# Kernel tuning notes

Hardware: AMD Instinct MI355X
Metric: run time of the kernel (lower is better)

Reference implementation:

```python
import jax, jax.numpy as jnp
import numpy as np

COMMITMENT = 0.25
THRESHOLD = 0.6
SNR_DB = 30.0  # eval_snr_db default-ish channel condition (fixed for determinism)
LN_EPS = 1e-5


def _layernorm(x, g, b):
    m = jnp.mean(x, axis=-1, keepdims=True)
    v = jnp.var(x, axis=-1, keepdims=True)
    return (x - m) * jax.lax.rsqrt(v + LN_EPS) * g + b


def _vq(x, codebook):
    # x: [T, D], codebook: [K, D]. Nearest-neighbor quantize + per-token VQ loss + STE.
    d = (x * x).sum(-1, keepdims=True) - 2.0 * (x @ codebook.T) + (codebook * codebook).sum(-1)  # [T, K]
    idx = jnp.argmin(d, axis=-1)
    q = codebook[idx]  # [T, D]
    loss = (COMMITMENT * jnp.mean((x - jax.lax.stop_gradient(q)) ** 2, axis=-1)
            + jnp.mean((jax.lax.stop_gradient(x) - q) ** 2, axis=-1))  # [T]
    q_ste = x + jax.lax.stop_gradient(q - x)
    return q_ste, loss


def setup_inputs() -> dict:
    key = jax.random.key(0)
    ks = jax.random.split(key, 8)
    B, N, De, Dq, Dd = 64, 196, 768, 512, 256
    return {
        'x_tokens': jax.random.normal(ks[0], (B, N, De), jnp.float32),
        'fim_logits': jax.random.normal(ks[1], (B, N, 1), jnp.float32),
        'W_proj': jax.random.normal(ks[2], (De, Dq), jnp.float32) * (1.0 / np.sqrt(De)),
        'b_proj': jnp.zeros((Dq,), jnp.float32),
        'ln_g': jnp.ones((Dq,), jnp.float32),
        'ln_b': jnp.zeros((Dq,), jnp.float32),
        'cb_high': jax.random.normal(ks[3], (4096, Dq), jnp.float32),
        'cb_low': jax.random.normal(ks[4], (256, Dq), jnp.float32),
        'W_dec': jax.random.normal(ks[5], (Dq, Dd), jnp.float32) * (1.0 / np.sqrt(Dq)),
        'b_dec': jnp.zeros((Dd,), jnp.float32),
        'h_ri': jax.random.normal(ks[6], (B, 2), jnp.float32),
        'noise': jax.random.normal(ks[7], (B, N, Dq), jnp.float32),
    }


def reference(x_tokens, fim_logits, W_proj, b_proj, ln_g, ln_b, cb_high, cb_low, W_dec, b_dec, h_ri, noise):
    B, N, _ = x_tokens.shape
    score = jax.nn.sigmoid(fim_logits[..., 0])          # [B, N]
    route_high = score > THRESHOLD                       # [B, N] bool

    x_proj = _layernorm(x_tokens @ W_proj + b_proj, ln_g, ln_b)  # [B, N, Dq]
    D = x_proj.shape[-1]
    xf = x_proj.reshape(-1, D)
    mf = route_high.reshape(-1)
    sf = score.reshape(-1)

    # Compute both experts densely, select with mask (same math as the masked
    # gather/scatter dispatch in the torch code, jit-friendly static shapes).
    q_high, loss_high = _vq(xf, cb_high)
    q_low, loss_low = _vq(xf, cb_low)
    final = jnp.where(mf[:, None], q_high, q_low).reshape(B, N, D)

    n_high = jnp.maximum(mf.sum(), 1)
    n_low = jnp.maximum((~mf).sum(), 1)
    vq_loss = (jnp.sum(jnp.where(mf, loss_high * sf, 0.0)) / n_high
               + jnp.sum(jnp.where(mf, 0.0, loss_low * (1.0 - sf))) / n_low) / 2.0

    # Rayleigh channel: per-sample fading magnitude h = |CN(0,1)|/sqrt(2), AWGN, equalize.
    n_var = 10.0 ** (-SNR_DB / 10.0)
    h = jnp.sqrt((h_ri ** 2).sum(-1)) / jnp.sqrt(2.0)    # [B]
    h = h[:, None, None]
    y = (h * final + jnp.sqrt(n_var) * noise) / h

    x_dec = y @ W_dec + b_dec                            # [B, N, 256]
    return x_dec, vq_loss
```

## Files before the change

kernel.cpp:

```cpp
#include <hip/hip_runtime.h>
#include <math.h>

#define T_TOK 12544
#define DE 768
#define DQ 512
#define DD 256
#define SEQ 196
#define NCH 4096
#define NCL 256
#define SPL_H 16
#define CODES_PER_BLK 256
#define MARGIN 2.0f
#define CAND_CAP 16
#define VQTOK 32

typedef __attribute__((ext_vector_type(8))) short s16x8;
typedef __attribute__((ext_vector_type(4))) float f32x4;

__device__ __forceinline__ float wave_reduce_sum(float v) {
    #pragma unroll
    for (int off = 32; off > 0; off >>= 1) v += __shfl_xor(v, off);
    return v;
}

__device__ __forceinline__ unsigned short f2bf(float f) {
    unsigned int u = __float_as_uint(f);
    u = (u + 0x7fffu + ((u >> 16) & 1u)) >> 16;
    return (unsigned short)u;
}
__device__ __forceinline__ float bf2f(unsigned short h) {
    return __uint_as_float(((unsigned int)h) << 16);
}

__device__ __forceinline__ void gload_lds16(const unsigned short* g, unsigned short* l) {
    __builtin_amdgcn_global_load_lds(
        (const __attribute__((address_space(1))) void*)g,
        (__attribute__((address_space(3))) void*)l,
        16, 0, 0);
}

__device__ __forceinline__ void sumsq_body(const float* __restrict__ cb,
                                           float* __restrict__ cs2,
                                           unsigned short* __restrict__ cbB,
                                           int blk, int NC) {
    int row = blk * 4 + (threadIdx.x >> 6);
    int lane = threadIdx.x & 63;
    if (row >= NC) return;
    const float4* p = (const float4*)(cb + (size_t)row * DQ);
    float4 a = p[lane];
    float4 b = p[lane + 64];
    if (cbB) {
        unsigned short* dst = cbB + (size_t)row * DQ;
        ushort4 ha, hb;
        ha.x = f2bf(a.x); ha.y = f2bf(a.y); ha.z = f2bf(a.z); ha.w = f2bf(a.w);
        hb.x = f2bf(b.x); hb.y = f2bf(b.y); hb.z = f2bf(b.z); hb.w = f2bf(b.w);
        *(ushort4*)(dst + lane * 4) = ha;
        *(ushort4*)(dst + 256 + lane * 4) = hb;
    }
    float s = a.x*a.x + a.y*a.y + a.z*a.z + a.w*a.w
            + b.x*b.x + b.y*b.y + b.z*b.z + b.w*b.w;
    s = wave_reduce_sum(s);
    if (lane == 0) cs2[row] = s;
}

__device__ __forceinline__ void split_body(const float* __restrict__ W, int K, int N,
                                           unsigned short* __restrict__ Thi,
                                           unsigned short* __restrict__ Tlo,
                                           int blk, int nb) {
    int total = K * N;
    for (int idx = blk * 256 + threadIdx.x; idx < total; idx += nb * 256) {
        int n = idx / K, k = idx - n * K;
        float v = W[(size_t)k * N + n];
        unsigned short h = f2bf(v);
        Thi[idx] = h;
        Tlo[idx] = f2bf(v - bf2f(h));
    }
}

__global__ __launch_bounds__(256) void prep_all(const float* __restrict__ cb_h,
                                                float* __restrict__ cs2h,
                                                unsigned short* __restrict__ cbhB,
                                                const float* __restrict__ cb_l,
                                                float* __restrict__ cs2l,
                                                unsigned short* __restrict__ cblB,
                                                const float* __restrict__ Wp,
                                                unsigned short* __restrict__ WThi,
                                                unsigned short* __restrict__ WTlo,
                                                const float* __restrict__ Wd,
                                                unsigned short* __restrict__ WdThi,
                                                unsigned short* __restrict__ WdTlo,
                                                int* __restrict__ counts) {
    int blk = blockIdx.x;
    if (blk == 0 && threadIdx.x == 0) { counts[0] = 0; counts[1] = 0; }
    if (blk < 1024)       sumsq_body(cb_h, cs2h, cbhB, blk, NCH);
    else if (blk < 1088)  sumsq_body(cb_l, cs2l, cblB, blk - 1024, NCL);
    else if (blk < 1600)  split_body(Wp, DE, DQ, WThi, WTlo, blk - 1088, 512);
    else                  split_body(Wd, DQ, DD, WdThi, WdTlo, blk - 1600, 256);
}

template<int NC>
__global__ __launch_bounds__(256) void code_sumsq(const float* __restrict__ cb,
                                                  float* __restrict__ cs2) {
    sumsq_body(cb, cs2, nullptr, blockIdx.x, NC);
}

template<int KDIM, int NSTRIDE>
__global__ __launch_bounds__(256) void gemm_mfma3_128(const float* __restrict__ A,
                                                      const unsigned short* __restrict__ BThi,
                                                      const unsigned short* __restrict__ BTlo,
                                                      const float* __restrict__ bias,
                                                      float* __restrict__ out) {
    __shared__ __align__(16) unsigned short Ahi[128 * 32];
    __shared__ __align__(16) unsigned short Alo[128 * 32];
    __shared__ __align__(16) unsigned short Bhi[128 * 32];
    __shared__ __align__(16) unsigned short Blo[128 * 32];
    const int m0 = blockIdx.x * 128, n0 = blockIdx.y * 128;
    const int tid = threadIdx.x, lane = tid & 63, w = tid >> 6;
    const int wr = w >> 1, wc = w & 1;
    const int arow = tid >> 1, ahalf = tid & 1;

    const int cb0 = w * 2, cb1 = w * 2 + 1;
    const int gcol0 = n0 + cb0 * 16 + (lane >> 2);
    const int gcol1 = n0 + cb1 * 16 + (lane >> 2);
    const int ch0 = (lane & 3) ^ ((gcol0 >> 1) & 3);
    const int ch1 = (lane & 3) ^ ((gcol1 >> 1) & 3);
    const unsigned short* sH0 = BThi + (size_t)gcol0 * KDIM + ch0 * 8;
    const unsigned short* sH1 = BThi + (size_t)gcol1 * KDIM + ch1 * 8;
    const unsigned short* sL0 = BTlo + (size_t)gcol0 * KDIM + ch0 * 8;
    const unsigned short* sL1 = BTlo + (size_t)gcol1 * KDIM + ch1 * 8;

    f32x4 acc[4][4] = {};
    const int NT = KDIM / 32;
    for (int t = 0; t < NT; t++) {
        const int k0 = t * 32;
        gload_lds16(sH0 + k0, Bhi + cb0 * 512);
        gload_lds16(sH1 + k0, Bhi + cb1 * 512);
        gload_lds16(sL0 + k0, Blo + cb0 * 512);
        gload_lds16(sL1 + k0, Blo + cb1 * 512);
        {
            const float* src = A + (size_t)(m0 + arow) * KDIM + k0 + ahalf * 16;
            float4 v0 = *(const float4*)(src + 0);
            float4 v1 = *(const float4*)(src + 4);
            float4 v2 = *(const float4*)(src + 8);
            float4 v3 = *(const float4*)(src + 12);
            float xv[16] = {v0.x,v0.y,v0.z,v0.w, v1.x,v1.y,v1.z,v1.w,
                            v2.x,v2.y,v2.z,v2.w, v3.x,v3.y,v3.z,v3.w};
            const int swzA = (arow >> 1) & 3;
            #pragma unroll
            for (int cc = 0; cc < 2; cc++) {
                unsigned int hw[4], lw[4];
                #pragma unroll
                for (int j = 0; j < 4; j++) {
                    float f0 = xv[cc*8 + 2*j], f1 = xv[cc*8 + 2*j + 1];
                    unsigned short h0 = f2bf(f0), h1 = f2bf(f1);
                    unsigned short l0 = f2bf(f0 - bf2f(h0));
                    unsigned short l1 = f2bf(f1 - bf2f(h1));
                    hw[j] = (unsigned)h0 | ((unsigned)h1 << 16);
                    lw[j] = (unsigned)l0 | ((unsigned)l1 << 16);
                }
                int c = ahalf * 2 + cc;
                int doff = arow * 32 + (c ^ swzA) * 8;
                *(uint4*)&Ahi[doff] = make_uint4(hw[0], hw[1], hw[2], hw[3]);
                *(uint4*)&Alo[doff] = make_uint4(lw[0], lw[1], lw[2], lw[3]);
            }
        }
        __syncthreads();
        const int fr = lane & 15, fs = lane >> 4;
        s16x8 ah[4], al[4];
        #pragma unroll
        for (int tm = 0; tm < 4; tm++) {
            int row = wr * 64 + tm * 16 + fr;
            int off = row * 32 + (fs ^ ((row >> 1) & 3)) * 8;
            ah[tm] = *(const s16x8*)&Ahi[off];
            al[tm] = *(const s16x8*)&Alo[off];
        }
        #pragma unroll
        for (int tn = 0; tn < 4; tn++) {
            int col = wc * 64 + tn * 16 + fr;
            int boff = col * 32 + (fs ^ ((col >> 1) & 3)) * 8;
            s16x8 bh = *(const s16x8*)&Bhi[boff];
            s16x8 bl = *(const s16x8*)&Blo[boff];
            #pragma unroll
            for (int tm = 0; tm < 4; tm++) {
                acc[tm][tn] = __builtin_amdgcn_mfma_f32_16x16x32_bf16(ah[tm], bh, acc[tm][tn], 0, 0, 0);
                acc[tm][tn] = __builtin_amdgcn_mfma_f32_16x16x32_bf16(ah[tm], bl, acc[tm][tn], 0, 0, 0);
                acc[tm][tn] = __builtin_amdgcn_mfma_f32_16x16x32_bf16(al[tm], bh, acc[tm][tn], 0, 0, 0);
            }
        }
        __syncthreads();
    }
    const int fr = lane & 15, fg = lane >> 4;
    #pragma unroll
    for (int tn = 0; tn < 4; tn++) {
        const int col = n0 + wc * 64 + tn * 16 + fr;
        const float bb = bias[col];
        #pragma unroll
        for (int tm = 0; tm < 4; tm++) {
            #pragma unroll
            for (int r = 0; r < 4; r++) {
                int row = m0 + wr * 64 + tm * 16 + fg * 4 + r;
                out[(size_t)row * NSTRIDE + col] = acc[tm][tn][r] + bb;
            }
        }
    }
}

__global__ __launch_bounds__(256) void dec_mfma3_loss(const float* __restrict__ A,
                                                      const unsigned short* __restrict__ BThi,
                                                      const unsigned short* __restrict__ BTlo,
                                                      const float* __restrict__ bias,
                                                      float* __restrict__ out,
                                                      const float* __restrict__ lh,
                                                      const float* __restrict__ ll,
                                                      const int* __restrict__ counts) {
    __shared__ __align__(16) unsigned short Ahi[2][64 * 32];
    __shared__ __align__(16) unsigned short Alo[2][64 * 32];
    __shared__ __align__(16) unsigned short Bhi[2][64 * 32];
    __shared__ __align__(16) unsigned short Blo[2][64 * 32];
    if (blockIdx.x == T_TOK / 64) {
        if (blockIdx.y != 0) return;
        float* sh = (float*)&Ahi[0][0];
        float* sl = sh + 256;
        int tid = threadIdx.x;
        float ah = 0.f, al = 0.f;
        for (int t = tid; t < T_TOK; t += 256) { ah += lh[t]; al += ll[t]; }
        sh[tid] = ah; sl[tid] = al;
        __syncthreads();
        for (int o = 128; o > 0; o >>= 1) {
            if (tid < o) { sh[tid] += sh[tid + o]; sl[tid] += sl[tid + o]; }
            __syncthreads();
        }
        if (tid == 0) {
            int nh = counts[0];
            int nl = T_TOK - nh;
            nh = nh > 1 ? nh : 1;
            nl = nl > 1 ? nl : 1;
            out[(size_t)T_TOK * DD] = 0.5f * (sh[0] / (float)nh + sl[0] / (float)nl);
        }
        return;
    }
    const int m0 = blockIdx.x * 64, n0 = blockIdx.y * 64;
    const int tid = threadIdx.x, lane = tid & 63, w = tid >> 6;
    const int stok = tid >> 2, sslot = tid & 3;

    f32x4 acc[4] = {};
    float4 av0, av1;
    uint4 bh4, bl4;

    auto loadStep = [&](int k0) {
        const float* src = A + (size_t)(m0 + stok) * DQ + k0 + sslot * 8;
        av0 = *(const float4*)src;
        av1 = *(const float4*)(src + 4);
        size_t soff = (size_t)(n0 + stok) * DQ + k0 + sslot * 8;
        bh4 = *(const uint4*)(BThi + soff);
        bl4 = *(const uint4*)(BTlo + soff);
    };
    auto writeStep = [&](int buf) {
        float xv[8] = {av0.x, av0.y, av0.z, av0.w, av1.x, av1.y, av1.z, av1.w};
        unsigned int hw[4], lw[4];
        #pragma unroll
        for (int j = 0; j < 4; j++) {
            unsigned short h0 = f2bf(xv[2*j]),   h1 = f2bf(xv[2*j+1]);
            unsigned short l0 = f2bf(xv[2*j] - bf2f(h0));
            unsigned short l1 = f2bf(xv[2*j+1] - bf2f(h1));
            hw[j] = (unsigned)h0 | ((unsigned)h1 << 16);
            lw[j] = (unsigned)l0 | ((unsigned)l1 << 16);
        }
        int doffA = stok * 32 + (sslot ^ ((stok >> 1) & 3)) * 8;
        *(uint4*)&Ahi[buf][doffA] = make_uint4(hw[0], hw[1], hw[2], hw[3]);
        *(uint4*)&Alo[buf][doffA] = make_uint4(lw[0], lw[1], lw[2], lw[3]);
        *(uint4*)&Bhi[buf][doffA] = bh4;
        *(uint4*)&Blo[buf][doffA] = bl4;
    };

    loadStep(0); writeStep(0); __syncthreads();
    const int NT = DQ / 32;
    for (int t = 0; t < NT; t++) {
        const int cur = t & 1;
        if (t + 1 < NT) loadStep((t + 1) * 32);
        const int fr = lane & 15, fs = lane >> 4;
        s16x8 ah[4], al[4];
        #pragma unroll
        for (int tm = 0; tm < 4; tm++) {
            int tok = tm * 16 + fr;
            int off = tok * 32 + (fs ^ ((tok >> 1) & 3)) * 8;
            ah[tm] = *(const s16x8*)&Ahi[cur][off];
            al[tm] = *(const s16x8*)&Alo[cur][off];
        }
        {
            int col = w * 16 + fr;
            int boff = col * 32 + (fs ^ ((col >> 1) & 3)) * 8;
            s16x8 bh = *(const s16x8*)&Bhi[cur][boff];
            s16x8 bl = *(const s16x8*)&Blo[cur][boff];
            #pragma unroll
            for (int tm = 0; tm < 4; tm++) {
                acc[tm] = __builtin_amdgcn_mfma_f32_16x16x32_bf16(ah[tm], bh, acc[tm], 0, 0, 0);
                acc[tm] = __builtin_amdgcn_mfma_f32_16x16x32_bf16(ah[tm], bl, acc[tm], 0, 0, 0);
                acc[tm] = __builtin_amdgcn_mfma_f32_16x16x32_bf16(al[tm], bh, acc[tm], 0, 0, 0);
            }
        }
        if (t + 1 < NT) writeStep(cur ^ 1);
        __syncthreads();
    }
    const int fr = lane & 15, fg = lane >> 4;
    {
        const int col = n0 + w * 16 + fr;
        const float bb = bias[col];
        #pragma unroll
        for (int tm = 0; tm < 4; tm++) {
            #pragma unroll
            for (int r = 0; r < 4; r++) {
                int row = m0 + tm * 16 + fg * 4 + r;
                out[(size_t)row * DD + col] = acc[tm][r] + bb;
            }
        }
    }
}

__global__ __launch_bounds__(256) void proj_gemm(const float* __restrict__ X,
                                                 const float* __restrict__ W,
                                                 const float* __restrict__ bias,
                                                 float* __restrict__ out) {
    __shared__ float As[32][66];
    __shared__ float Bs[32][64];
    const int m0 = blockIdx.x * 64, n0 = blockIdx.y * 64;
    const int tid = threadIdx.x;
    const int tx = tid & 15, ty = tid >> 4;
    float acc[4][4] = {};
    for (int k0 = 0; k0 < DE; k0 += 32) {
        {
            int e = tid;
            int r = e >> 3, c4 = e & 7;
            float4 v = *(const float4*)(X + (size_t)(m0 + r) * DE + k0 + c4 * 4);
            As[c4*4+0][r] = v.x; As[c4*4+1][r] = v.y; As[c4*4+2][r] = v.z; As[c4*4+3][r] = v.w;
            e = tid + 256;
            r = e >> 3; c4 = e & 7;
            v = *(const float4*)(X + (size_t)(m0 + r) * DE + k0 + c4 * 4);
            As[c4*4+0][r] = v.x; As[c4*4+1][r] = v.y; As[c4*4+2][r] = v.z; As[c4*4+3][r] = v.w;
        }
        {
            int e = tid;
            int kk = e >> 4, c4 = e & 15;
            *(float4*)&Bs[kk][c4*4] = *(const float4*)(W + (size_t)(k0 + kk) * DQ + n0 + c4 * 4);
            e = tid + 256;
            kk = e >> 4; c4 = e & 15;
            *(float4*)&Bs[kk][c4*4] = *(const float4*)(W + (size_t)(k0 + kk) * DQ + n0 + c4 * 4);
        }
        __syncthreads();
        #pragma unroll
        for (int k = 0; k < 32; k++) {
            float2 a01 = *(const float2*)&As[k][ty * 4];
            float2 a23 = *(const float2*)&As[k][ty * 4 + 2];
            float4 b = *(const float4*)&Bs[k][tx * 4];
            float av[4] = {a01.x, a01.y, a23.x, a23.y};
            float bv[4] = {b.x, b.y, b.z, b.w};
            #pragma unroll
            for (int i = 0; i < 4; i++)
                #pragma unroll
                for (int j = 0; j < 4; j++)
                    acc[i][j] += av[i] * bv[j];
        }
        __syncthreads();
    }
    float4 bv4 = *(const float4*)(bias + n0 + tx * 4);
    float bb[4] = {bv4.x, bv4.y, bv4.z, bv4.w};
    #pragma unroll
    for (int i = 0; i < 4; i++) {
        int row = m0 + ty * 4 + i;
        float4 o;
        o.x = acc[i][0] + bb[0];
        o.y = acc[i][1] + bb[1];
        o.z = acc[i][2] + bb[2];
        o.w = acc[i][3] + bb[3];
        *(float4*)(out + (size_t)row * DQ + n0 + tx * 4) = o;
    }
}

__global__ __launch_bounds__(256) void ln_route_compact(float* __restrict__ xp,
                                                        const float* __restrict__ g,
                                                        const float* __restrict__ b,
                                                        const float* __restrict__ logits,
                                                        float* __restrict__ score,
                                                        unsigned short* __restrict__ xpB,
                                                        int* __restrict__ hlist,
                                                        int* __restrict__ llist,
                                                        int* __restrict__ counts) {
    __shared__ int hloc[32], lloc[32];
    __shared__ int nh_s, nl_s, bh_s, bl_s;
    const int tid = threadIdx.x, lane = tid & 63, wv = tid >> 6;
    if (tid == 0) { nh_s = 0; nl_s = 0; }
    __syncthreads();
    float4 g0 = *(const float4*)(g + lane * 4);
    float4 g1 = *(const float4*)(g + 256 + lane * 4);
    float4 b0 = *(const float4*)(b + lane * 4);
    float4 b1 = *(const float4*)(b + 256 + lane * 4);
    const int rbase = blockIdx.x * 32 + wv * 8;
    for (int i = 0; i < 8; i++) {
        int row = rbase + i;
        float* p = xp + (size_t)row * DQ;
        float4 v0 = *(float4*)(p + lane * 4);
        float4 v1 = *(float4*)(p + 256 + lane * 4);
        float s  = v0.x + v0.y + v0.z + v0.w + v1.x + v1.y + v1.z + v1.w;
        float ss = v0.x*v0.x + v0.y*v0.y + v0.z*v0.z + v0.w*v0.w
                 + v1.x*v1.x + v1.y*v1.y + v1.z*v1.z + v1.w*v1.w;
        s = wave_reduce_sum(s);
        ss = wave_reduce_sum(ss);
        float m = s * (1.f / DQ);
        float var = ss * (1.f / DQ) - m * m;
        float scale = rsqrtf(var + 1e-5f);
        float4 o0, o1;
        o0.x = (v0.x - m) * scale * g0.x + b0.x;
        o0.y = (v0.y - m) * scale * g0.y + b0.y;
        o0.z = (v0.z - m) * scale * g0.z + b0.z;
        o0.w = (v0.w - m) * scale * g0.w + b0.w;
        o1.x = (v1.x - m) * scale * g1.x + b1.x;
        o1.y = (v1.y - m) * scale * g1.y + b1.y;
        o1.z = (v1.z - m) * scale * g1.z + b1.z;
        o1.w = (v1.w - m) * scale * g1.w + b1.w;
        *(float4*)(p + lane * 4) = o0;
        *(float4*)(p + 256 + lane * 4) = o1;
        unsigned short* dst = xpB + (size_t)row * DQ;
        ushort4 h0, h1;
        h0.x = f2bf(o0.x); h0.y = f2bf(o0.y); h0.z = f2bf(o0.z); h0.w = f2bf(o0.w);
        h1.x = f2bf(o1.x); h1.y = f2bf(o1.y); h1.z = f2bf(o1.z); h1.w = f2bf(o1.w);
        *(ushort4*)(dst + lane * 4) = h0;
        *(ushort4*)(dst + 256 + lane * 4) = h1;
        if (lane == 0) {
            float lg = logits[row];
            float sc = 1.f / (1.f + expf(-lg));
            score[row] = sc;
            if (sc > 0.6f) { int pp = atomicAdd(&nh_s, 1); hloc[pp] = row; }
            else           { int pp = atomicAdd(&nl_s, 1); lloc[pp] = row; }
        }
    }
    __syncthreads();
    if (tid == 0) {
        bh_s = atomicAdd(&counts[0], nh_s);
        bl_s = atomicAdd(&counts[1], nl_s);
    }
    __syncthreads();
    if (tid < 32) {
        if (tid < nh_s) hlist[bh_s + tid] = hloc[tid];
    } else if (tid < 64) {
        int j = tid - 32;
        if (j < nl_s) llist[bl_s + j] = lloc[j];
    }
}

__global__ __launch_bounds__(256) void ln_route(float* __restrict__ xp,
                                                const float* __restrict__ g,
                                                const float* __restrict__ b,
                                                const float* __restrict__ logits,
                                                float* __restrict__ score,
                                                int* __restrict__ mask,
                                                unsigned short* __restrict__ xpB) {
    int row = blockIdx.x * 4 + (threadIdx.x >> 6);
    int lane = threadIdx.x & 63;
    float* p = xp + (size_t)row * DQ;
    float4 v0 = *(float4*)(p + lane * 4);
    float4 v1 = *(float4*)(p + 256 + lane * 4);
    float s  = v0.x + v0.y + v0.z + v0.w + v1.x + v1.y + v1.z + v1.w;
    float ss = v0.x*v0.x + v0.y*v0.y + v0.z*v0.z + v0.w*v0.w
             + v1.x*v1.x + v1.y*v1.y + v1.z*v1.z + v1.w*v1.w;
    s = wave_reduce_sum(s);
    ss = wave_reduce_sum(ss);
    float m = s * (1.f / DQ);
    float var = ss * (1.f / DQ) - m * m;
    float scale = rsqrtf(var + 1e-5f);
    float4 g0 = *(const float4*)(g + lane * 4);
    float4 g1 = *(const float4*)(g + 256 + lane * 4);
    float4 b0 = *(const float4*)(b + lane * 4);
    float4 b1 = *(const float4*)(b + 256 + lane * 4);
    float4 o0, o1;
    o0.x = (v0.x - m) * scale * g0.x + b0.x;
    o0.y = (v0.y - m) * scale * g0.y + b0.y;
    o0.z = (v0.z - m) * scale * g0.z + b0.z;
    o0.w = (v0.w - m) * scale * g0.w + b0.w;
    o1.x = (v1.x - m) * scale * g1.x + b1.x;
    o1.y = (v1.y - m) * scale * g1.y + b1.y;
    o1.z = (v1.z - m) * scale * g1.z + b1.z;
    o1.w = (v1.w - m) * scale * g1.w + b1.w;
    *(float4*)(p + lane * 4) = o0;
    *(float4*)(p + 256 + lane * 4) = o1;
    if (xpB) {
        unsigned short* dst = xpB + (size_t)row * DQ;
        ushort4 h0, h1;
        h0.x = f2bf(o0.x); h0.y = f2bf(o0.y); h0.z = f2bf(o0.z); h0.w = f2bf(o0.w);
        h1.x = f2bf(o1.x); h1.y = f2bf(o1.y); h1.z = f2bf(o1.z); h1.w = f2bf(o1.w);
        *(ushort4*)(dst + lane * 4) = h0;
        *(ushort4*)(dst + 256 + lane * 4) = h1;
    }
    if (lane == 0) {
        float lg = logits[row];
        float sc = 1.f / (1.f + expf(-lg));
        score[row] = sc;
        mask[row] = sc > 0.6f ? 1 : 0;
    }
}

__global__ __launch_bounds__(1024) void scan_compact(const int* __restrict__ mask,
                                                     int* __restrict__ hlist,
                                                     int* __restrict__ llist,
                                                     int* __restrict__ counts) {
    __shared__ int wsum[16];
    __shared__ int base_h, base_l;
    int tid = threadIdx.x, lane = tid & 63, wid = tid >> 6;
    if (tid == 0) { base_h = 0; base_l = 0; }
    __syncthreads();
    for (int t0 = 0; t0 < T_TOK; t0 += 1024) {
        int t = t0 + tid;
        int valid = t < T_TOK;
        int m = valid ? mask[t] : 0;
        unsigned long long bal = __ballot(m);
        int pre = __popcll(bal & ((1ull << lane) - 1ull));
        if (lane == 0) wsum[wid] = __popcll(bal);
        __syncthreads();
        int woff = 0;
        for (int w = 0; w < wid; w++) woff += wsum[w];
        int btot = 0;
        for (int w = 0; w < 16; w++) btot += wsum[w];
        int vcnt = T_TOK - t0; if (vcnt > 1024) vcnt = 1024;
        int bh = base_h, bl = base_l;
        if (valid) {
            if (m) hlist[bh + woff + pre] = t;
            else   llist[bl + (tid - (woff + pre))] = t;
        }
        __syncthreads();
        if (tid == 0) { base_h = bh + btot; base_l = bl + (vcnt - btot); }
        __syncthreads();
    }
    if (tid == 0) { counts[0] = base_h; counts[1] = base_l; }
}

__global__ __launch_bounds__(256) void vq_mfma_all(const unsigned short* __restrict__ xpB,
                                                   const unsigned short* __restrict__ cbhB,
                                                   const float* __restrict__ cs2h,
                                                   const int* __restrict__ hlist,
                                                   const unsigned short* __restrict__ cblB,
                                                   const float* __restrict__ cs2l,
                                                   const int* __restrict__ llist,
                                                   const int* __restrict__ counts,
                                                   float* __restrict__ smaxH,
                                                   int* __restrict__ scntH,
                                                   uint2* __restrict__ candH,
                                                   float* __restrict__ smaxL,
                                                   int* __restrict__ scntL,
                                                   uint2* __restrict__ candL) {
    const int by = blockIdx.y;
    const unsigned short* cbB; const float* cs2; const int* list;
    float* smax; int* scnt; uint2* cand;
    int count, slice, SPLIT;
    if (by < SPL_H) {
        cbB = cbhB; cs2 = cs2h; list = hlist; count = counts[0];
        slice = by; SPLIT = SPL_H; smax = smaxH; scnt = scntH; cand = candH;
    } else {
        cbB = cblB; cs2 = cs2l; list = llist; count = counts[1];
        slice = 0; SPLIT = 1; smax = smaxL; scnt = scntL; cand = candL;
    }
    const int base = blockIdx.x * VQTOK;
    if (base >= count) return;
    const int cbase = slice * CODES_PER_BLK;

    __shared__ __align__(16) unsigned short Abuf[VQTOK * 32];
    __shared__ __align__(16) unsigned short Bbuf[256 * 32];
    __shared__ float wmaxs[4][VQTOK];
    __shared__ float tokmax[VQTOK];
    __shared__ int ccnt[VQTOK];
    __shared__ uint2 cland[VQTOK][CAND_CAP];
    __shared__ int rows_s[VQTOK];

    const int tid = threadIdx.x;
    const int lane = tid & 63;
    const int w = tid >> 6;
    const int stok = tid >> 2, sslot = tid & 3;

    if (tid < VQTOK) {
        int tl = base + tid;
        rows_s[tid] = list[tl < count ? tl : (count - 1)];
        ccnt[tid] = 0;
    }
    __syncthreads();

    const int swz = sslot ^ ((stok >> 1) & 3);
    const unsigned short* gA  = xpB + (size_t)rows_s[stok & (VQTOK - 1)] * DQ + swz * 8;
    const unsigned short* gB0 = cbB + (size_t)(cbase + 0 * 64 + stok) * DQ + swz * 8;
    const unsigned short* gB1 = cbB + (size_t)(cbase + 1 * 64 + stok) * DQ + swz * 8;
    const unsigned short* gB2 = cbB + (size_t)(cbase + 2 * 64 + stok) * DQ + swz * 8;
    const unsigned short* gB3 = cbB + (size_t)(cbase + 3 * 64 + stok) * DQ + swz * 8;
    unsigned short* dA = Abuf + w * 512;
    unsigned short* dB = Bbuf + w * 512;

    f32x4 acc[2][4] = {};

    const int NT = DQ / 32;
    for (int t = 0; t < NT; t++) {
        const int k0 = t * 32;
        if (w < 2) gload_lds16(gA + k0, dA);
        gload_lds16(gB0 + k0, dB + 0 * 2048);
        gload_lds16(gB1 + k0, dB + 1 * 2048);
        gload_lds16(gB2 + k0, dB + 2 * 2048);
        gload_lds16(gB3 + k0, dB + 3 * 2048);
        __syncthreads();
        const int fr = lane & 15, fs = lane >> 4;
        s16x8 af[2], bf[4];
        #pragma unroll
        for (int tm = 0; tm < 2; tm++) {
            int tok = tm * 16 + fr;
            af[tm] = *(const s16x8*)&Abuf[tok * 32 + (fs ^ ((tok >> 1) & 3)) * 8];
        }
        #pragma unroll
        for (int tn = 0; tn < 4; tn++) {
            int cl = w * 64 + tn * 16 + fr;
            bf[tn] = *(const s16x8*)&Bbuf[cl * 32 + (fs ^ ((cl >> 1) & 3)) * 8];
        }
        #pragma unroll
        for (int tm = 0; tm < 2; tm++)
            #pragma unroll
            for (int tn = 0; tn < 4; tn++)
                acc[tm][tn] = __builtin_amdgcn_mfma_f32_16x16x32_bf16(af[tm], bf[tn], acc[tm][tn], 0, 0, 0);
        __syncthreads();
    }

    const int fr = lane & 15, fg = lane >> 4;
    float c2[4];
    #pragma unroll
    for (int tn = 0; tn < 4; tn++) c2[tn] = 0.5f * cs2[cbase + w * 64 + tn * 16 + fr];

    #pragma unroll
    for (int tm = 0; tm < 2; tm++) {
        #pragma unroll
        for (int r = 0; r < 4; r++) {
            float m4 = -3.0e38f;
            #pragma unroll
            for (int tn = 0; tn < 4; tn++) {
                float s = acc[tm][tn][r] - c2[tn];
                m4 = fmaxf(m4, s);
            }
            #pragma unroll
            for (int off = 1; off < 16; off <<= 1)
                m4 = fmaxf(m4, __shfl_xor(m4, off));
            if (fr == 0) wmaxs[w][tm * 16 + fg * 4 + r] = m4;
        }
    }
    __syncthreads();
    if (tid < VQTOK)
        tokmax[tid] = fmaxf(fmaxf(wmaxs[0][tid], wmaxs[1][tid]),
                            fmaxf(wmaxs[2][tid], wmaxs[3][tid]));
    __syncthreads();

    #pragma unroll
    for (int tm = 0; tm < 2; tm++) {
        #pragma unroll
        for (int r = 0; r < 4; r++) {
            int token = tm * 16 + fg * 4 + r;
            float thr = tokmax[token] - MARGIN;
            #pragma unroll
            for (int tn = 0; tn < 4; tn++) {
                float s = acc[tm][tn][r] - c2[tn];
                if (s > thr) {
                    int pos = atomicAdd(&ccnt[token], 1);
                    if (pos < CAND_CAP) {
                        uint2 cd;
                        cd.x = __float_as_uint(s);
                        cd.y = (unsigned)(cbase + w * 64 + tn * 16 + fr);
                        cland[token][pos] = cd;
                    }
                }
            }
        }
    }
    __syncthreads();

    if (tid < VQTOK) {
        int tl = base + tid;
        if (tl < count) {
            smax[(size_t)tl * SPLIT + slice] = tokmax[tid];
            scnt[(size_t)tl * SPLIT + slice] = min(ccnt[tid], CAND_CAP);
        }
    }
    for (int i = tid; i < VQTOK * CAND_CAP; i += 256) {
        int token = i >> 4, j = i & (CAND_CAP - 1);
        int tl = base + token;
        if (tl < count && j < min(ccnt[token], CAND_CAP))
            cand[((size_t)tl * SPLIT + slice) * CAND_CAP + j] = cland[token][j];
    }
}

__global__ __launch_bounds__(256) void vq_rescore_all(float* __restrict__ xp,
                                                      const float* __restrict__ cb_h,
                                                      const float* __restrict__ smaxH,
                                                      const int* __restrict__ scntH,
                                                      const uint2* __restrict__ candH,
                                                      const int* __restrict__ hlist,
                                                      const float* __restrict__ cb_l,
                                                      const float* __restrict__ smaxL,
                                                      const int* __restrict__ scntL,
                                                      const uint2* __restrict__ candL,
                                                      const int* __restrict__ llist,
                                                      const int* __restrict__ counts,
                                                      int* __restrict__ out_idx,
                                                      const float* __restrict__ noise,
                                                      const float* __restrict__ h_ri,
                                                      const float* __restrict__ score,
                                                      float* __restrict__ lh,
                                                      float* __restrict__ ll) {
    const int HB = T_TOK / 4;
    int bx = blockIdx.x;
    const float* cb; const float* smax; const int* scnt; const uint2* cand; const int* list;
    int count, SPLIT, cidx;
    if (bx < HB) {
        cb = cb_h; smax = smaxH; scnt = scntH; cand = candH; list = hlist;
        count = counts[0]; SPLIT = SPL_H; cidx = 0;
    } else {
        bx -= HB;
        cb = cb_l; smax = smaxL; scnt = scntL; cand = candL; list = llist;
        count = counts[1]; SPLIT = 1; cidx = 1;
    }
    const int wid = threadIdx.x >> 6;
    const int lane = threadIdx.x & 63;
    const int tl = bx * 4 + wid;
    if (tl >= count) return;

    float gm = -3.0e38f;
    if (lane < SPLIT) gm = smax[(size_t)tl * SPLIT + lane];
    #pragma unroll
    for (int off = 1; off < 64; off <<= 1)
        gm = fmaxf(gm, __shfl_xor(gm, off));
    const float thr = gm - MARGIN;

    const int t = list[tl];
    float xv[8];
    #pragma unroll
    for (int kk = 0; kk < 8; kk++) xv[kk] = xp[(size_t)t * DQ + lane * 8 + kk];

    double bs = -1.0e300;
    int bi = 0x7fffffff;
    for (int s = 0; s < SPLIT; s++) {
        int cn = scnt[(size_t)tl * SPLIT + s];
        for (int j = 0; j < cn; j++) {
            uint2 cd = cand[((size_t)tl * SPLIT + s) * CAND_CAP + j];
            float av = __uint_as_float(cd.x);
            if (av >= thr) {
                int code = (int)cd.y;
                const float* crow = cb + (size_t)code * DQ;
                double dot = 0.0, nrm = 0.0;
                #pragma unroll
                for (int kk = 0; kk < 8; kk++) {
                    double cv = (double)crow[lane * 8 + kk];
                    dot += (double)xv[kk] * cv;
                    nrm += cv * cv;
                }
                #pragma unroll
                for (int off = 1; off < 64; off <<= 1) {
                    dot += __shfl_xor(dot, off);
                    nrm += __shfl_xor(nrm, off);
                }
                double sc = dot - 0.5 * nrm;
                if (sc > bs || (sc == bs && code < bi)) { bs = sc; bi = code; }
            }
        }
    }
    const float* qrow = cb + (size_t)bi * DQ;
    float4 q0 = *(const float4*)(qrow + lane * 8);
    float4 q1 = *(const float4*)(qrow + lane * 8 + 4);
    const float* nz = noise + (size_t)t * DQ;
    float4 n0 = *(const float4*)(nz + lane * 8);
    float4 n1 = *(const float4*)(nz + lane * 8 + 4);
    float ds = 0.f, dx;
    dx = xv[0] - q0.x; ds += dx * dx;
    dx = xv[1] - q0.y; ds += dx * dx;
    dx = xv[2] - q0.z; ds += dx * dx;
    dx = xv[3] - q0.w; ds += dx * dx;
    dx = xv[4] - q1.x; ds += dx * dx;
    dx = xv[5] - q1.y; ds += dx * dx;
    dx = xv[6] - q1.z; ds += dx * dx;
    dx = xv[7] - q1.w; ds += dx * dx;
    ds = wave_reduce_sum(ds);
    int bbt = t / SEQ;
    float hh0 = h_ri[bbt * 2], hh1 = h_ri[bbt * 2 + 1];
    float hh = sqrtf((hh0 * hh0 + hh1 * hh1) * 0.5f);
    float cc = sqrtf(1e-3f) / hh;
    float4 y0, y1;
    y0.x = q0.x + cc * n0.x; y0.y = q0.y + cc * n0.y;
    y0.z = q0.z + cc * n0.z; y0.w = q0.w + cc * n0.w;
    y1.x = q1.x + cc * n1.x; y1.y = q1.y + cc * n1.y;
    y1.z = q1.z + cc * n1.z; y1.w = q1.w + cc * n1.w;
    *(float4*)(xp + (size_t)t * DQ + lane * 8) = y0;
    *(float4*)(xp + (size_t)t * DQ + lane * 8 + 4) = y1;
    if (lane == 0) {
        out_idx[t] = bi;
        float loss = 1.25f * ds * (1.f / DQ);
        float sc = score[t];
        if (cidx == 0) { lh[t] = loss * sc;  ll[t] = 0.f; }
        else           { lh[t] = 0.f;        ll[t] = loss * (1.f - sc); }
    }
}

template<int NC, int SPLIT>
__global__ __launch_bounds__(256) void vq_partial(const float* __restrict__ xp,
                                                  const float* __restrict__ cb,
                                                  const float* __restrict__ cs2,
                                                  const int* __restrict__ list,
                                                  const int* __restrict__ counts,
                                                  int cidx,
                                                  float* __restrict__ part_s,
                                                  int* __restrict__ part_i) {
    const int count = counts[cidx];
    const int base = blockIdx.x * 64;
    if (base >= count) return;
    const int CODES = NC / SPLIT;
    const int cbase = blockIdx.y * CODES;
    __shared__ float As[32][68];
    __shared__ float Cs[32][68];
    __shared__ int rows_s[64];
    const int tid = threadIdx.x;
    if (tid < 64) {
        int tl = base + tid;
        rows_s[tid] = list[tl < count ? tl : (count - 1)];
    }
    __syncthreads();
    const int tx = tid & 15, ty = tid >> 4;
    float best_s[4];
    int best_i[4];
    #pragma unroll
    for (int i = 0; i < 4; i++) { best_s[i] = -3.0e38f; best_i[i] = 0; }
    for (int c0 = cbase; c0 < cbase + CODES; c0 += 64) {
        float acc[4][4] = {};
        for (int k0 = 0; k0 < DQ; k0 += 32) {
            {
                int e = tid;
                int r = e >> 3, c4 = e & 7;
                float4 v = *(const float4*)(xp + (size_t)rows_s[r] * DQ + k0 + c4 * 4);
                As[c4*4+0][r] = v.x; As[c4*4+1][r] = v.y; As[c4*4+2][r] = v.z; As[c4*4+3][r] = v.w;
                e = tid + 256; r = e >> 3; c4 = e & 7;
                v = *(const float4*)(xp + (size_t)rows_s[r] * DQ + k0 + c4 * 4);
                As[c4*4+0][r] = v.x; As[c4*4+1][r] = v.y; As[c4*4+2][r] = v.z; As[c4*4+3][r] = v.w;
            }
            {
                int e = tid;
                int r = e >> 3, c4 = e & 7;
                float4 v = *(const float4*)(cb + (size_t)(c0 + r) * DQ + k0 + c4 * 4);
                Cs[c4*4+0][r] = v.x; Cs[c4*4+1][r] = v.y; Cs[c4*4+2][r] = v.z; Cs[c4*4+3][r] = v.w;
                e = tid + 256; r = e >> 3; c4 = e & 7;
                v = *(const float4*)(cb + (size_t)(c0 + r) * DQ + k0 + c4 * 4);
                Cs[c4*4+0][r] = v.x; Cs[c4*4+1][r] = v.y; Cs[c4*4+2][r] = v.z; Cs[c4*4+3][r] = v.w;
            }
            __syncthreads();
            #pragma unroll
            for (int k = 0; k < 32; k++) {
                float4 a = *(const float4*)&As[k][ty * 4];
                float4 b = *(const float4*)&Cs[k][tx * 4];
                float av[4] = {a.x, a.y, a.z, a.w};
                float bv[4] = {b.x, b.y, b.z, b.w};
                #pragma unroll
                for (int i = 0; i < 4; i++)
                    #pragma unroll
                    for (int j = 0; j < 4; j++)
                        acc[i][j] += av[i] * bv[j];
            }
            __syncthreads();
        }
        float4 c2v = *(const float4*)(cs2 + c0 + tx * 4);
        float c2[4] = {c2v.x, c2v.y, c2v.z, c2v.w};
        #pragma unroll
        for (int i = 0; i < 4; i++) {
            float s = acc[i][0] - 0.5f * c2[0];
            int bi = c0 + tx * 4;
            #pragma unroll
            for (int j = 1; j < 4; j++) {
                float sj = acc[i][j] - 0.5f * c2[j];
                if (sj > s) { s = sj; bi = c0 + tx * 4 + j; }
            }
            #pragma unroll
            for (int off = 1; off < 16; off <<= 1) {
                float os = __shfl_xor(s, off);
                int oi = __shfl_xor(bi, off);
                if (os > s || (os == s && oi < bi)) { s = os; bi = oi; }
            }
            if (s > best_s[i] || (s == best_s[i] && bi < best_i[i])) {
                best_s[i] = s; best_i[i] = bi;
            }
        }
    }
    if (tx == 0) {
        #pragma unroll
        for (int i = 0; i < 4; i++) {
            int tl = base + ty * 4 + i;
            if (tl < count) {
                part_s[(size_t)tl * SPLIT + blockIdx.y] = best_s[i];
                part_i[(size_t)tl * SPLIT + blockIdx.y] = best_i[i];
            }
        }
    }
}

template<int SPLIT>
__global__ __launch_bounds__(256) void vq_reduce(const float* __restrict__ part_s,
                                                 const int* __restrict__ part_i,
                                                 const int* __restrict__ list,
                                                 const int* __restrict__ counts,
                                                 int cidx,
                                                 int* __restrict__ out_idx) {
    int tl = blockIdx.x * 256 + threadIdx.x;
    if (tl >= counts[cidx]) return;
    float bs = part_s[(size_t)tl * SPLIT];
    int bi = part_i[(size_t)tl * SPLIT];
    #pragma unroll
    for (int s = 1; s < SPLIT; s++) {
        float v = part_s[(size_t)tl * SPLIT + s];
        int vi = part_i[(size_t)tl * SPLIT + s];
        if (v > bs || (v == bs && vi < bi)) { bs = v; bi = vi; }
    }
    out_idx[list[tl]] = bi;
}

__global__ __launch_bounds__(256) void gather_loss_y(float* __restrict__ xp,
                                                     const float* __restrict__ cb_h,
                                                     const float* __restrict__ cb_l,
                                                     const int* __restrict__ idx,
                                                     const float* __restrict__ score,
                                                     const int* __restrict__ mask,
                                                     const float* __restrict__ noise,
                                                     const float* __restrict__ h_ri,
                                                     float* __restrict__ lh,
                                                     float* __restrict__ ll) {
    int t = blockIdx.x * 4 + (threadIdx.x >> 6);
    int lane = threadIdx.x & 63;
    int m = mask[t];
    float sc = score[t];
    const float* q = (m ? cb_h : cb_l) + (size_t)idx[t] * DQ;
    float* x = xp + (size_t)t * DQ;
    const float* nz = noise + (size_t)t * DQ;
    int bb = t / SEQ;
    float h0 = h_ri[bb * 2], h1 = h_ri[bb * 2 + 1];
    float h = sqrtf((h0 * h0 + h1 * h1) * 0.5f);
    float c = sqrtf(1e-3f) / h;
    float4 xv0 = *(float4*)(x + lane * 4);
    float4 xv1 = *(float4*)(x + 256 + lane * 4);
    float4 qv0 = *(const float4*)(q + lane * 4);
    float4 qv1 = *(const float4*)(q + 256 + lane * 4);
    float4 nv0 = *(const float4*)(nz + lane * 4);
    float4 nv1 = *(const float4*)(nz + 256 + lane * 4);
    float dx, ds = 0.f;
    dx = xv0.x - qv0.x; ds += dx * dx;
    dx = xv0.y - qv0.y; ds += dx * dx;
    dx = xv0.z - qv0.z; ds += dx * dx;
    dx = xv0.w - qv0.w; ds += dx * dx;
    dx = xv1.x - qv1.x; ds += dx * dx;
    dx = xv1.y - qv1.y; ds += dx * dx;
    dx = xv1.z - qv1.z; ds += dx * dx;
    dx = xv1.w - qv1.w; ds += dx * dx;
    ds = wave_reduce_sum(ds);
    float4 y0, y1;
    y0.x = qv0.x + c * nv0.x; y0.y = qv0.y + c * nv0.y;
    y0.z = qv0.z + c * nv0.z; y0.w = qv0.w + c * nv0.w;
    y1.x = qv1.x + c * nv1.x; y1.y = qv1.y + c * nv1.y;
    y1.z = qv1.z + c * nv1.z; y1.w = qv1.w + c * nv1.w;
    *(float4*)(x + lane * 4) = y0;
    *(float4*)(x + 256 + lane * 4) = y1;
    if (lane == 0) {
        float loss = 1.25f * ds * (1.f / DQ);
        lh[t] = m ? loss * sc : 0.f;
        ll[t] = m ? 0.f : loss * (1.f - sc);
    }
}

__global__ __launch_bounds__(256) void loss_reduce(const float* __restrict__ lh,
                                                   const float* __restrict__ ll,
                                                   const int* __restrict__ counts,
                                                   float* __restrict__ out) {
    __shared__ float sh[256], sl[256];
    int tid = threadIdx.x;
    float ah = 0.f, al = 0.f;
    for (int t = tid; t < T_TOK; t += 256) { ah += lh[t]; al += ll[t]; }
    sh[tid] = ah; sl[tid] = al;
    __syncthreads();
    for (int o = 128; o > 0; o >>= 1) {
        if (tid < o) { sh[tid] += sh[tid + o]; sl[tid] += sl[tid + o]; }
        __syncthreads();
    }
    if (tid == 0) {
        int nh = counts[0];
        int nl = T_TOK - nh;
        nh = nh > 1 ? nh : 1;
        nl = nl > 1 ? nl : 1;
        out[(size_t)T_TOK * DD] = 0.5f * (sh[0] / (float)nh + sl[0] / (float)nl);
    }
}

__global__ __launch_bounds__(256) void dec_gemm(const float* __restrict__ Y,
                                                const float* __restrict__ W,
                                                const float* __restrict__ bias,
                                                float* __restrict__ out) {
    __shared__ float As[32][66];
    __shared__ float Bs[32][64];
    const int m0 = blockIdx.x * 64, n0 = blockIdx.y * 64;
    const int tid = threadIdx.x;
    const int tx = tid & 15, ty = tid >> 4;
    float acc[4][4] = {};
    for (int k0 = 0; k0 < DQ; k0 += 32) {
        {
            int e = tid;
            int r = e >> 3, c4 = e & 7;
            float4 v = *(const float4*)(Y + (size_t)(m0 + r) * DQ + k0 + c4 * 4);
            As[c4*4+0][r] = v.x; As[c4*4+1][r] = v.y; As[c4*4+2][r] = v.z; As[c4*4+3][r] = v.w;
            e = tid + 256; r = e >> 3; c4 = e & 7;
            v = *(const float4*)(Y + (size_t)(m0 + r) * DQ + k0 + c4 * 4);
            As[c4*4+0][r] = v.x; As[c4*4+1][r] = v.y; As[c4*4+2][r] = v.z; As[c4*4+3][r] = v.w;
        }
        {
            int e = tid;
            int kk = e >> 4, c4 = e & 15;
            *(float4*)&Bs[kk][c4*4] = *(const float4*)(W + (size_t)(k0 + kk) * DD + n0 + c4 * 4);
            e = tid + 256; kk = e >> 4; c4 = e & 15;
            *(float4*)&Bs[kk][c4*4] = *(const float4*)(W + (size_t)(k0 + kk) * DD + n0 + c4 * 4);
        }
        __syncthreads();
        #pragma unroll
        for (int k = 0; k < 32; k++) {
            float2 a01 = *(const float2*)&As[k][ty * 4];
            float2 a23 = *(const float2*)&As[k][ty * 4 + 2];
            float4 b = *(const float4*)&Bs[k][tx * 4];
            float av[4] = {a01.x, a01.y, a23.x, a23.y};
            float bv[4] = {b.x, b.y, b.z, b.w};
            #pragma unroll
            for (int i = 0; i < 4; i++)
                #pragma unroll
                for (int j = 0; j < 4; j++)
                    acc[i][j] += av[i] * bv[j];
        }
        __syncthreads();
    }
    float4 bv4 = *(const float4*)(bias + n0 + tx * 4);
    float bbv[4] = {bv4.x, bv4.y, bv4.z, bv4.w};
    #pragma unroll
    for (int i = 0; i < 4; i++) {
        int row = m0 + ty * 4 + i;
        float4 o;
        o.x = acc[i][0] + bbv[0];
        o.y = acc[i][1] + bbv[1];
        o.z = acc[i][2] + bbv[2];
        o.w = acc[i][3] + bbv[3];
        *(float4*)(out + (size_t)row * DD + n0 + tx * 4) = o;
    }
}

extern "C" void kernel_launch(void* const* d_in, const int* in_sizes, int n_in,
                              void* d_out, int out_size, void* d_ws, size_t ws_size,
                              hipStream_t stream) {
    const float* x_tokens = (const float*)d_in[0];
    const float* fim      = (const float*)d_in[1];
    const float* W_proj   = (const float*)d_in[2];
    const float* b_proj   = (const float*)d_in[3];
    const float* ln_g     = (const float*)d_in[4];
    const float* ln_b     = (const float*)d_in[5];
    const float* cb_high  = (const float*)d_in[6];
    const float* cb_low   = (const float*)d_in[7];
    const float* W_dec    = (const float*)d_in[8];
    const float* b_dec    = (const float*)d_in[9];
    const float* h_ri     = (const float*)d_in[10];
    const float* noise    = (const float*)d_in[11];
    float* out = (float*)d_out;

    char* ws = (char*)d_ws;
    size_t off = 0;
    float* xp = (float*)(ws + off);     off += (size_t)T_TOK * DQ * 4;
    int*   idxb = (int*)(ws + off);     off += (size_t)T_TOK * 4;
    float* score = (float*)(ws + off);  off += (size_t)T_TOK * 4;
    int*   mask = (int*)(ws + off);     off += (size_t)T_TOK * 4;
    float* lh = (float*)(ws + off);     off += (size_t)T_TOK * 4;
    float* ll = (float*)(ws + off);     off += (size_t)T_TOK * 4;
    int*   hlist = (int*)(ws + off);    off += (size_t)T_TOK * 4;
    int*   llist = (int*)(ws + off);    off += (size_t)T_TOK * 4;
    int*   counts = (int*)(ws + off);   off += 64;
    float* cs2h = (float*)(ws + off);   off += (size_t)NCH * 4;
    float* cs2l = (float*)(ws + off);   off += (size_t)NCL * 4;
    size_t off_common = off;

    unsigned short* xpB  = (unsigned short*)(ws + off); off += (size_t)T_TOK * DQ * 2;
    unsigned short* cbhB = (unsigned short*)(ws + off); off += (size_t)NCH * DQ * 2;
    unsigned short* cblB = (unsigned short*)(ws + off); off += (size_t)NCL * DQ * 2;
    float* smaxH = (float*)(ws + off);  off += (size_t)T_TOK * SPL_H * 4;
    int*   scntH = (int*)(ws + off);    off += (size_t)T_TOK * SPL_H * 4;
    uint2* candH = (uint2*)(ws + off);  off += (size_t)T_TOK * SPL_H * CAND_CAP * 8;
    float* smaxL = (float*)(ws + off);  off += (size_t)T_TOK * 4;
    int*   scntL = (int*)(ws + off);    off += (size_t)T_TOK * 4;
    uint2* candL = (uint2*)(ws + off);  off += (size_t)T_TOK * CAND_CAP * 8;
    unsigned short* WThi  = (unsigned short*)(ws + off); off += (size_t)DQ * DE * 2;
    unsigned short* WTlo  = (unsigned short*)(ws + off); off += (size_t)DQ * DE * 2;
    unsigned short* WdThi = (unsigned short*)(ws + off); off += (size_t)DD * DQ * 2;
    unsigned short* WdTlo = (unsigned short*)(ws + off); off += (size_t)DD * DQ * 2;
    size_t need_new = off;
    const bool use_mfma = ws_size >= need_new;

    if (use_mfma) {
        prep_all<<<1856, 256, 0, stream>>>(cb_high, cs2h, cbhB, cb_low, cs2l, cblB,
                                           W_proj, WThi, WTlo, W_dec, WdThi, WdTlo, counts);
        gemm_mfma3_128<DE, DQ><<<dim3(T_TOK / 128, DQ / 128), 256, 0, stream>>>(
            x_tokens, WThi, WTlo, b_proj, xp);
        ln_route_compact<<<T_TOK / 32, 256, 0, stream>>>(
            xp, ln_g, ln_b, fim, score, xpB, hlist, llist, counts);
        vq_mfma_all<<<dim3(T_TOK / VQTOK, SPL_H + 1), 256, 0, stream>>>(
            xpB, cbhB, cs2h, hlist, cblB, cs2l, llist, counts,
            smaxH, scntH, candH, smaxL, scntL, candL);
        vq_rescore_all<<<2 * (T_TOK / 4), 256, 0, stream>>>(
            xp, cb_high, smaxH, scntH, candH, hlist,
            cb_low, smaxL, scntL, candL, llist,
            counts, idxb, noise, h_ri, score, lh, ll);
        dec_mfma3_loss<<<dim3(T_TOK / 64 + 1, DD / 64), 256, 0, stream>>>(
            xp, WdThi, WdTlo, b_dec, out, lh, ll, counts);
    } else {
        code_sumsq<NCH><<<NCH / 4, 256, 0, stream>>>(cb_high, cs2h);
        code_sumsq<NCL><<<NCL / 4, 256, 0, stream>>>(cb_low, cs2l);
        proj_gemm<<<dim3(T_TOK / 64, DQ / 64), 256, 0, stream>>>(x_tokens, W_proj, b_proj, xp);
        ln_route<<<T_TOK / 4, 256, 0, stream>>>(xp, ln_g, ln_b, fim, score, mask, nullptr);
        scan_compact<<<1, 1024, 0, stream>>>(mask, hlist, llist, counts);
        float* part_s = (float*)(ws + off_common);
        int*   part_i = (int*)(ws + off_common + (size_t)T_TOK * 16 * 4);
        vq_partial<NCH, 16><<<dim3(T_TOK / 64, 16), 256, 0, stream>>>(
            xp, cb_high, cs2h, hlist, counts, 0, part_s, part_i);
        vq_reduce<16><<<(T_TOK + 255) / 256, 256, 0, stream>>>(part_s, part_i, hlist, counts, 0, idxb);
        vq_partial<NCL, 4><<<dim3(T_TOK / 64, 4), 256, 0, stream>>>(
            xp, cb_low, cs2l, llist, counts, 1, part_s, part_i);
        vq_reduce<4><<<(T_TOK + 255) / 256, 256, 0, stream>>>(part_s, part_i, llist, counts, 1, idxb);
        gather_loss_y<<<T_TOK / 4, 256, 0, stream>>>(xp, cb_high, cb_low, idxb, score, mask,
                                                     noise, h_ri, lh, ll);
        loss_reduce<<<1, 256, 0, stream>>>(lh, ll, counts, out);
        dec_gemm<<<dim3(T_TOK / 64, DD / 64), 256, 0, stream>>>(xp, W_dec, b_dec, out);
    }
}
```

Baseline: 198.4 us.

## Enlarge VQ MFMA token tile to 128 with 512-thread 2x4 wave layout

Raises the VQ distance kernel's token tile from 32 to 128 tokens per block and moves to 512 threads arranged as 2x4 waves, each computing a 64-token x 64-code subtile. Each codebook tile loaded into LDS is now reused across four times as many tokens, which cuts global/L2 traffic on the codebook and the number of blocks. In exchange each wave holds more accumulator registers, LDS use per block grows, and there are fewer blocks, so occupancy may drop and more tail tokens may be wasted.

```diff
diff --git a/kernel.cpp b/kernel.cpp
--- a/kernel.cpp
+++ b/kernel.cpp
@@ -12,7 +12,7 @@
 #define CODES_PER_BLK 256
 #define MARGIN 2.0f
 #define CAND_CAP 16
-#define VQTOK 32
+#define VQTOK 128
 
 typedef __attribute__((ext_vector_type(8))) short s16x8;
 typedef __attribute__((ext_vector_type(4))) float f32x4;
@@ -532,7 +532,7 @@
     if (tid == 0) { counts[0] = base_h; counts[1] = base_l; }
 }
 
-__global__ __launch_bounds__(256) void vq_mfma_all(const unsigned short* __restrict__ xpB,
+__global__ __launch_bounds__(512) void vq_mfma_all(const unsigned short* __restrict__ xpB,
                                                    const unsigned short* __restrict__ cbhB,
                                                    const float* __restrict__ cs2h,
                                                    const int* __restrict__ hlist,
@@ -563,7 +563,7 @@
 
     __shared__ __align__(16) unsigned short Abuf[VQTOK * 32];
     __shared__ __align__(16) unsigned short Bbuf[256 * 32];
-    __shared__ float wmaxs[4][VQTOK];
+    __shared__ float wmaxs[8][64];
     __shared__ float tokmax[VQTOK];
     __shared__ int ccnt[VQTOK];
     __shared__ uint2 cland[VQTOK][CAND_CAP];
@@ -572,6 +572,7 @@
     const int tid = threadIdx.x;
     const int lane = tid & 63;
     const int w = tid >> 6;
+    const int wr = w >> 2, wc = w & 3;
     const int stok = tid >> 2, sslot = tid & 3;
 
     if (tid < VQTOK) {
@@ -582,39 +583,36 @@
     __syncthreads();
 
     const int swz = sslot ^ ((stok >> 1) & 3);
-    const unsigned short* gA  = xpB + (size_t)rows_s[stok & (VQTOK - 1)] * DQ + swz * 8;
-    const unsigned short* gB0 = cbB + (size_t)(cbase + 0 * 64 + stok) * DQ + swz * 8;
-    const unsigned short* gB1 = cbB + (size_t)(cbase + 1 * 64 + stok) * DQ + swz * 8;
-    const unsigned short* gB2 = cbB + (size_t)(cbase + 2 * 64 + stok) * DQ + swz * 8;
-    const unsigned short* gB3 = cbB + (size_t)(cbase + 3 * 64 + stok) * DQ + swz * 8;
-    unsigned short* dA = Abuf + w * 512;
-    unsigned short* dB = Bbuf + w * 512;
-
-    f32x4 acc[2][4] = {};
+    const unsigned short* gA  = xpB + (size_t)rows_s[stok] * DQ + swz * 8;
+    const unsigned short* gB0 = cbB + (size_t)(cbase + stok) * DQ + swz * 8;
+    const unsigned short* gB1 = cbB + (size_t)(cbase + 128 + stok) * DQ + swz * 8;
+    unsigned short* dA  = Abuf + w * 512;
+    unsigned short* dB0 = Bbuf + w * 512;
+    unsigned short* dB1 = Bbuf + 128 * 32 + w * 512;
+
+    f32x4 acc[4][4] = {};
 
     const int NT = DQ / 32;
     for (int t = 0; t < NT; t++) {
         const int k0 = t * 32;
-        if (w < 2) gload_lds16(gA + k0, dA);
-        gload_lds16(gB0 + k0, dB + 0 * 2048);
-        gload_lds16(gB1 + k0, dB + 1 * 2048);
-        gload_lds16(gB2 + k0, dB + 2 * 2048);
-        gload_lds16(gB3 + k0, dB + 3 * 2048);
+        gload_lds16(gA  + k0, dA);
+        gload_lds16(gB0 + k0, dB0);
+        gload_lds16(gB1 + k0, dB1);
         __syncthreads();
         const int fr = lane & 15, fs = lane >> 4;
-        s16x8 af[2], bf[4];
-        #pragma unroll
-        for (int tm = 0; tm < 2; tm++) {
-            int tok = tm * 16 + fr;
+        s16x8 af[4], bf[4];
+        #pragma unroll
+        for (int tm = 0; tm < 4; tm++) {
+            int tok = wr * 64 + tm * 16 + fr;
             af[tm] = *(const s16x8*)&Abuf[tok * 32 + (fs ^ ((tok >> 1) & 3)) * 8];
         }
         #pragma unroll
         for (int tn = 0; tn < 4; tn++) {
-            int cl = w * 64 + tn * 16 + fr;
+            int cl = wc * 64 + tn * 16 + fr;
             bf[tn] = *(const s16x8*)&Bbuf[cl * 32 + (fs ^ ((cl >> 1) & 3)) * 8];
         }
         #pragma unroll
-        for (int tm = 0; tm < 2; tm++)
+        for (int tm = 0; tm < 4; tm++)
             #pragma unroll
             for (int tn = 0; tn < 4; tn++)
                 acc[tm][tn] = __builtin_amdgcn_mfma_f32_16x16x32_bf16(af[tm], bf[tn], acc[tm][tn], 0, 0, 0);
@@ -624,10 +622,10 @@
     const int fr = lane & 15, fg = lane >> 4;
     float c2[4];
     #pragma unroll
-    for (int tn = 0; tn < 4; tn++) c2[tn] = 0.5f * cs2[cbase + w * 64 + tn * 16 + fr];
+    for (int tn = 0; tn < 4; tn++) c2[tn] = 0.5f * cs2[cbase + wc * 64 + tn * 16 + fr];
 
     #pragma unroll
-    for (int tm = 0; tm < 2; tm++) {
+    for (int tm = 0; tm < 4; tm++) {
         #pragma unroll
         for (int r = 0; r < 4; r++) {
             float m4 = -3.0e38f;
@@ -643,16 +641,18 @@
         }
     }
     __syncthreads();
-    if (tid < VQTOK)
-        tokmax[tid] = fmaxf(fmaxf(wmaxs[0][tid], wmaxs[1][tid]),
-                            fmaxf(wmaxs[2][tid], wmaxs[3][tid]));
+    if (tid < VQTOK) {
+        int wrt = tid >> 6, tlc = tid & 63;
+        tokmax[tid] = fmaxf(fmaxf(wmaxs[wrt * 4 + 0][tlc], wmaxs[wrt * 4 + 1][tlc]),
+                            fmaxf(wmaxs[wrt * 4 + 2][tlc], wmaxs[wrt * 4 + 3][tlc]));
+    }
     __syncthreads();
 
     #pragma unroll
-    for (int tm = 0; tm < 2; tm++) {
+    for (int tm = 0; tm < 4; tm++) {
         #pragma unroll
         for (int r = 0; r < 4; r++) {
-            int token = tm * 16 + fg * 4 + r;
+            int token = wr * 64 + tm * 16 + fg * 4 + r;
             float thr = tokmax[token] - MARGIN;
             #pragma unroll
             for (int tn = 0; tn < 4; tn++) {
@@ -662,7 +662,7 @@
                     if (pos < CAND_CAP) {
                         uint2 cd;
                         cd.x = __float_as_uint(s);
-                        cd.y = (unsigned)(cbase + w * 64 + tn * 16 + fr);
+                        cd.y = (unsigned)(cbase + wc * 64 + tn * 16 + fr);
                         cland[token][pos] = cd;
                     }
                 }
@@ -678,7 +678,7 @@
             scnt[(size_t)tl * SPLIT + slice] = min(ccnt[tid], CAND_CAP);
         }
     }
-    for (int i = tid; i < VQTOK * CAND_CAP; i += 256) {
+    for (int i = tid; i < VQTOK * CAND_CAP; i += 512) {
         int token = i >> 4, j = i & (CAND_CAP - 1);
         int tl = base + token;
         if (tl < count && j < min(ccnt[token], CAND_CAP))
@@ -1100,7 +1100,7 @@
             x_tokens, WThi, WTlo, b_proj, xp);
         ln_route_compact<<<T_TOK / 32, 256, 0, stream>>>(
             xp, ln_g, ln_b, fim, score, xpB, hlist, llist, counts);
-        vq_mfma_all<<<dim3(T_TOK / VQTOK, SPL_H + 1), 256, 0, stream>>>(
+        vq_mfma_all<<<dim3(T_TOK / VQTOK, SPL_H + 1), 512, 0, stream>>>(
             xpB, cbhB, cs2h, hlist, cblB, cs2l, llist, counts,
             smaxH, scntH, candH, smaxL, scntL, candL);
         vq_rescore_all<<<2 * (T_TOK / 4), 256, 0, stream>>>(
```

Measured after the change: 198.0 us. Within noise of the previous version (-0.2%).
